# Kernel optimization log

Measured on AMD Instinct MI355X. Metric: run time of the kernel, lower is better.

The kernel has to match this reference:

```python
import jax, jax.numpy as jnp
import numpy as np

EPS = 1e-16


def setup_inputs() -> dict:
    key = jax.random.key(0)
    ks = jax.random.split(key, 7)
    B, N, C = 4096, 2048, 128  # batch of heads, memory rows, memory cols
    k = jax.random.normal(ks[0], (B, C), dtype=jnp.float32)
    beta = jax.random.normal(ks[1], (B, 1), dtype=jnp.float32)
    g = jax.random.normal(ks[2], (B, 1), dtype=jnp.float32)
    s = jax.random.normal(ks[3], (B, 3), dtype=jnp.float32)
    gamma = jax.random.normal(ks[4], (B, 1), dtype=jnp.float32)
    w_prev = jax.random.uniform(ks[5], (B, N), dtype=jnp.float32)
    w_prev = w_prev / jnp.sum(w_prev, axis=1, keepdims=True)  # valid weighting
    M = jax.random.normal(ks[6], (N, C), dtype=jnp.float32)  # memory matrix
    return {"k": k, "beta": beta, "g": g, "s": s, "gamma": gamma,
            "w_prev": w_prev, "M": M}


def reference(k, beta, g, s, gamma, w_prev, M):
    # head activations
    beta = jax.nn.softplus(beta)            # [B,1] key strength > 0
    g = jax.nn.sigmoid(g)                   # [B,1] interpolation gate
    s = jax.nn.softmax(s, axis=-1)          # [B,3] shift distribution
    gamma = 1.0 + jax.nn.softplus(gamma)    # [B,1] sharpening >= 1

    # content addressing: cosine similarity k vs memory rows
    k_norm = jnp.linalg.norm(k, axis=-1, keepdims=True)          # [B,1]
    m_norm = jnp.linalg.norm(M, axis=-1, keepdims=True)          # [N,1]
    sim = jnp.einsum('bc,nc->bn', k, M) / (k_norm * m_norm.T + EPS)  # [B,N]
    w_c = jax.nn.softmax(beta * sim, axis=-1)                    # [B,N]

    # interpolation with previous weighting
    w_g = g * w_c + (1.0 - g) * w_prev                           # [B,N]

    # circular convolution with 3-tap shift kernel (shifts -1, 0, +1)
    w_tilde = (s[:, 0:1] * jnp.roll(w_g, 1, axis=1)
               + s[:, 1:2] * w_g
               + s[:, 2:3] * jnp.roll(w_g, -1, axis=1))          # [B,N]

    # sharpening
    w_sharp = w_tilde ** gamma
    w = w_sharp / (jnp.sum(w_sharp, axis=1, keepdims=True) + EPS)
    return w
```

## Files before the change

kernel.cpp:

```cpp
#include <hip/hip_runtime.h>
#include <math.h>

#define NN 2048
#define CC 128
#define ROWS 16
#define EPSF 1e-16f

typedef __attribute__((ext_vector_type(8))) short bf16x8;
typedef __attribute__((ext_vector_type(4))) float f32x4;

__device__ __forceinline__ float softplusf(float x) {
  return fmaxf(x, 0.0f) + log1pf(__expf(-fabsf(x)));
}

union U8 { uint u[4]; bf16x8 v; };

__device__ __forceinline__ void split8(float4 a, float4 b, bf16x8& hi,
                                       bf16x8& lo, float& sq) {
  float f[8] = {a.x, a.y, a.z, a.w, b.x, b.y, b.z, b.w};
  U8 H, L;
#pragma unroll
  for (int i = 0; i < 4; ++i) {
    float f0 = f[2 * i], f1 = f[2 * i + 1];
    sq += f0 * f0;
    sq += f1 * f1;
    uint u0 = __float_as_uint(f0), u1 = __float_as_uint(f1);
    uint m0 = u0 & 0xffff0000u, m1 = u1 & 0xffff0000u;
    float r0 = f0 - __uint_as_float(m0);
    float r1 = f1 - __uint_as_float(m1);
    H.u[i] = (u0 >> 16) | m1;
    L.u[i] = (__float_as_uint(r0) >> 16) | (__float_as_uint(r1) & 0xffff0000u);
  }
  hi = H.v;
  lo = L.v;
}

__global__ __launch_bounds__(256) void ntm_prep_kernel(
    const float* __restrict__ kptr, const float* __restrict__ beta_,
    const float* __restrict__ g_, const float* __restrict__ s_,
    const float* __restrict__ gamma_, const float* __restrict__ M,
    bf16x8* __restrict__ Mhf, bf16x8* __restrict__ Mlf,
    bf16x8* __restrict__ Khf, bf16x8* __restrict__ Klf,
    float* __restrict__ imn, float* __restrict__ zb, float* __restrict__ gvv,
    float* __restrict__ gmv, float* __restrict__ s0a, float* __restrict__ s1a,
    float* __restrict__ s2a) {
  const int bid = blockIdx.x;
  const int t = threadIdx.x;
  if (bid < 96) {
    const int lane = t & 63;
    const int wv = t >> 6;
    const int l15 = lane & 15;
    const int lg = lane >> 4;
    const bool isM = bid < 32;
    const int grp = (isM ? bid : bid - 32) * 4 + wv;
    const float* src = (isM ? M : kptr) + (grp * 16 + l15) * CC + lg * 8;
    bf16x8* dh = (isM ? Mhf : Khf) + (grp * 4) * 64 + lane;
    bf16x8* dl = (isM ? Mlf : Klf) + (grp * 4) * 64 + lane;
    float sq = 0.f;
#pragma unroll
    for (int ks = 0; ks < 4; ++ks) {
      float4 a0 = *(const float4*)(src + ks * 32);
      float4 a1 = *(const float4*)(src + ks * 32 + 4);
      bf16x8 h, l;
      split8(a0, a1, h, l, sq);
      dh[ks * 64] = h;
      dl[ks * 64] = l;
    }
    sq += __shfl_xor(sq, 16, 64);
    sq += __shfl_xor(sq, 32, 64);
    if (lg == 0) {
      const int row = grp * 16 + l15;
      if (isM) {
        imn[row] = 1.0f / sqrtf(sq);
      } else {
        zb[row] = softplusf(beta_[row]) / sqrtf(sq);
      }
    }
  } else {
    const int r = (bid - 96) * 256 + t;
    gvv[r] = 1.0f / (1.0f + __expf(-g_[r]));
    gmv[r] = 1.0f + softplusf(gamma_[r]);
    float sh0 = s_[3 * r], sh1 = s_[3 * r + 1], sh2 = s_[3 * r + 2];
    float shm = fmaxf(sh0, fmaxf(sh1, sh2));
    float e0 = __expf(sh0 - shm), e1 = __expf(sh1 - shm), e2 = __expf(sh2 - shm);
    float sden = 1.0f / (e0 + e1 + e2);
    s0a[r] = e0 * sden;
    s1a[r] = e1 * sden;
    s2a[r] = e2 * sden;
  }
}

__global__ __launch_bounds__(1024) void ntm_main_kernel(
    const float* __restrict__ w_prev, const bf16x8* __restrict__ Mhf,
    const bf16x8* __restrict__ Mlf, const bf16x8* __restrict__ Khf,
    const bf16x8* __restrict__ Klf, const float* __restrict__ imn,
    const float* __restrict__ zb, const float* __restrict__ gvv,
    const float* __restrict__ gmv, const float* __restrict__ s0a,
    const float* __restrict__ s1a, const float* __restrict__ s2a,
    float* __restrict__ out) {
  __shared__ float red[ROWS][16];
  __shared__ float edges[ROWS][16][2];

  const int t = threadIdx.x;
  const int lane = t & 63;
  const int w = __builtin_amdgcn_readfirstlane(t >> 6);
  const int l15 = lane & 15;
  const int lg = lane >> 4;
  const int bg = blockIdx.x;
  const int b0 = bg * ROWS;

  bf16x8 ah[4], al[4];
#pragma unroll
  for (int ks = 0; ks < 4; ++ks) {
    ah[ks] = Khf[(bg * 4 + ks) * 64 + lane];
    al[ks] = Klf[(bg * 4 + ks) * 64 + lane];
  }

  f32x4 accT[8];
  float imn_t[8];
#pragma unroll
  for (int tt = 0; tt < 8; ++tt) {
    const int gM = 8 * w + tt;
    f32x4 acc = {0.f, 0.f, 0.f, 0.f};
#pragma unroll
    for (int ks = 0; ks < 4; ++ks) {
      bf16x8 bh = Mhf[(gM * 4 + ks) * 64 + lane];
      bf16x8 bl = Mlf[(gM * 4 + ks) * 64 + lane];
      acc = __builtin_amdgcn_mfma_f32_16x16x32_bf16(ah[ks], bh, acc, 0, 0, 0);
      acc = __builtin_amdgcn_mfma_f32_16x16x32_bf16(al[ks], bh, acc, 0, 0, 0);
      acc = __builtin_amdgcn_mfma_f32_16x16x32_bf16(ah[ks], bl, acc, 0, 0, 0);
    }
    accT[tt] = acc;
    imn_t[tt] = imn[128 * w + 16 * tt + l15];
  }

#pragma unroll
  for (int q = 0; q < 4; ++q) {
    const int rr = lg * 4 + q;
    const float zbv = zb[b0 + rr];
    float rs = 0.f;
#pragma unroll
    for (int tt = 0; tt < 8; ++tt) {
      float e = __expf(accT[tt][q] * imn_t[tt] * zbv);
      accT[tt][q] = e;
      rs += e;
    }
    rs += __shfl_xor(rs, 1, 64);
    rs += __shfl_xor(rs, 2, 64);
    rs += __shfl_xor(rs, 4, 64);
    rs += __shfl_xor(rs, 8, 64);
    if (l15 == 0) red[rr][w] = rs;
  }
  __syncthreads();

#pragma unroll
  for (int q = 0; q < 4; ++q) {
    const int rr = lg * 4 + q;
    float4 p0 = *(const float4*)&red[rr][0];
    float4 p1 = *(const float4*)&red[rr][4];
    float4 p2 = *(const float4*)&red[rr][8];
    float4 p3 = *(const float4*)&red[rr][12];
    float tot = (p0.x + p0.y + p0.z + p0.w) + (p1.x + p1.y + p1.z + p1.w) +
                (p2.x + p2.y + p2.z + p2.w) + (p3.x + p3.y + p3.z + p3.w);
    const float gv = gvv[b0 + rr];
    const float ge = gv / tot;
    const float om = 1.0f - gv;
    const size_t rbase = (size_t)(b0 + rr) * NN + 128 * w + l15;
#pragma unroll
    for (int tt = 0; tt < 8; ++tt) {
      float wp = w_prev[rbase + 16 * tt];
      accT[tt][q] = ge * accT[tt][q] + om * wp;
    }
    if (l15 == 0) edges[rr][w][0] = accT[0][q];
    if (l15 == 15) edges[rr][w][1] = accT[7][q];
  }
  __syncthreads();

  const int tm = (lane & 48) | ((lane + 15) & 15);
  const int tp = (lane & 48) | ((lane + 1) & 15);
#pragma unroll
  for (int q = 0; q < 4; ++q) {
    const int rr = lg * 4 + q;
    const float sh0 = s0a[b0 + rr];
    const float sh1 = s1a[b0 + rr];
    const float sh2 = s2a[b0 + rr];
    const float gammav = gmv[b0 + rr];
    const float eL = edges[rr][(w + 15) & 15][1];
    const float eR = edges[rr][(w + 1) & 15][0];

    float sm[8], sp[8];
#pragma unroll
    for (int tt = 0; tt < 8; ++tt) {
      sm[tt] = __shfl(accT[tt][q], tm, 64);
      sp[tt] = __shfl(accT[tt][q], tp, 64);
    }
    float rs = 0.f;
#pragma unroll
    for (int tt = 0; tt < 8; ++tt) {
      float pv = (l15 == 0) ? ((tt == 0) ? eL : sm[tt - 1]) : sm[tt];
      float nx = (l15 == 15) ? ((tt == 7) ? eR : sp[tt + 1]) : sp[tt];
      float wt = sh0 * pv + sh1 * accT[tt][q] + sh2 * nx;
      float p = __expf(gammav * __logf(wt));
      accT[tt][q] = p;
      rs += p;
    }
    rs += __shfl_xor(rs, 1, 64);
    rs += __shfl_xor(rs, 2, 64);
    rs += __shfl_xor(rs, 4, 64);
    rs += __shfl_xor(rs, 8, 64);
    if (l15 == 0) red[rr][w] = rs;
  }
  __syncthreads();

#pragma unroll
  for (int q = 0; q < 4; ++q) {
    const int rr = lg * 4 + q;
    float4 p0 = *(const float4*)&red[rr][0];
    float4 p1 = *(const float4*)&red[rr][4];
    float4 p2 = *(const float4*)&red[rr][8];
    float4 p3 = *(const float4*)&red[rr][12];
    float tot = (p0.x + p0.y + p0.z + p0.w) + (p1.x + p1.y + p1.z + p1.w) +
                (p2.x + p2.y + p2.z + p2.w) + (p3.x + p3.y + p3.z + p3.w);
    const float pinv = 1.0f / (tot + EPSF);
    const size_t rbase = (size_t)(b0 + rr) * NN + 128 * w + l15;
#pragma unroll
    for (int tt = 0; tt < 8; ++tt) {
      out[rbase + 16 * tt] = accT[tt][q] * pinv;
    }
  }
}

__global__ __launch_bounds__(1024) void ntm_main_fallback(
    const float* __restrict__ kptr, const float* __restrict__ beta_,
    const float* __restrict__ g_, const float* __restrict__ s_,
    const float* __restrict__ gamma_, const float* __restrict__ w_prev,
    const float* __restrict__ Mptr, float* __restrict__ out) {
  __shared__ float red[ROWS][16];
  __shared__ float edges[ROWS][16][2];
  const int t = threadIdx.x;
  const int lane = t & 63;
  const int w = __builtin_amdgcn_readfirstlane(t >> 6);
  const int l15 = lane & 15;
  const int lg = lane >> 4;
  const int b0 = blockIdx.x * ROWS;

  const float* kr = kptr + (b0 + l15) * CC + lg * 8;
  bf16x8 ah[4], al[4];
  float ksq = 0.f;
#pragma unroll
  for (int ks = 0; ks < 4; ++ks) {
    float4 a0 = *(const float4*)(kr + ks * 32);
    float4 a1 = *(const float4*)(kr + ks * 32 + 4);
    split8(a0, a1, ah[ks], al[ks], ksq);
  }
  ksq += __shfl_xor(ksq, 16, 64);
  ksq += __shfl_xor(ksq, 32, 64);
  const float ikn_own = 1.0f / sqrtf(ksq);

  f32x4 accT[8];
  float imn[8];
#pragma unroll
  for (int tt = 0; tt < 8; ++tt) {
    const int n0t = 128 * w + 16 * tt;
    const float* mr = Mptr + (size_t)(n0t + l15) * CC + lg * 8;
    f32x4 acc = {0.f, 0.f, 0.f, 0.f};
    float msq = 0.f;
#pragma unroll
    for (int ks = 0; ks < 4; ++ks) {
      float4 m0 = *(const float4*)(mr + ks * 32);
      float4 m1 = *(const float4*)(mr + ks * 32 + 4);
      bf16x8 bh, bl;
      split8(m0, m1, bh, bl, msq);
      acc = __builtin_amdgcn_mfma_f32_16x16x32_bf16(ah[ks], bh, acc, 0, 0, 0);
      acc = __builtin_amdgcn_mfma_f32_16x16x32_bf16(al[ks], bh, acc, 0, 0, 0);
      acc = __builtin_amdgcn_mfma_f32_16x16x32_bf16(ah[ks], bl, acc, 0, 0, 0);
    }
    msq += __shfl_xor(msq, 16, 64);
    msq += __shfl_xor(msq, 32, 64);
    imn[tt] = 1.0f / sqrtf(msq);
    accT[tt] = acc;
  }

#pragma unroll
  for (int q = 0; q < 4; ++q) {
    const int rr = lg * 4 + q;
    const float zb = softplusf(beta_[b0 + rr]) * __shfl(ikn_own, rr, 64);
    float rs = 0.f;
#pragma unroll
    for (int tt = 0; tt < 8; ++tt) {
      float e = __expf(accT[tt][q] * imn[tt] * zb);
      accT[tt][q] = e;
      rs += e;
    }
    rs += __shfl_xor(rs, 1, 64);
    rs += __shfl_xor(rs, 2, 64);
    rs += __shfl_xor(rs, 4, 64);
    rs += __shfl_xor(rs, 8, 64);
    if (l15 == 0) red[rr][w] = rs;
  }
  __syncthreads();

#pragma unroll
  for (int q = 0; q < 4; ++q) {
    const int rr = lg * 4 + q;
    float4 p0 = *(const float4*)&red[rr][0];
    float4 p1 = *(const float4*)&red[rr][4];
    float4 p2 = *(const float4*)&red[rr][8];
    float4 p3 = *(const float4*)&red[rr][12];
    float tot = (p0.x + p0.y + p0.z + p0.w) + (p1.x + p1.y + p1.z + p1.w) +
                (p2.x + p2.y + p2.z + p2.w) + (p3.x + p3.y + p3.z + p3.w);
    const float gv = 1.0f / (1.0f + __expf(-g_[b0 + rr]));
    const float ge = gv / tot;
    const float om = 1.0f - gv;
    const size_t rbase = (size_t)(b0 + rr) * NN + 128 * w + l15;
#pragma unroll
    for (int tt = 0; tt < 8; ++tt) {
      float wp = w_prev[rbase + 16 * tt];
      accT[tt][q] = ge * accT[tt][q] + om * wp;
    }
    if (l15 == 0) edges[rr][w][0] = accT[0][q];
    if (l15 == 15) edges[rr][w][1] = accT[7][q];
  }
  __syncthreads();

  const int tm = (lane & 48) | ((lane + 15) & 15);
  const int tp = (lane & 48) | ((lane + 1) & 15);
#pragma unroll
  for (int q = 0; q < 4; ++q) {
    const int rr = lg * 4 + q;
    float sh0 = s_[3 * (b0 + rr)];
    float sh1 = s_[3 * (b0 + rr) + 1];
    float sh2 = s_[3 * (b0 + rr) + 2];
    float shm = fmaxf(sh0, fmaxf(sh1, sh2));
    float e0 = __expf(sh0 - shm), e1 = __expf(sh1 - shm), e2 = __expf(sh2 - shm);
    float sden = 1.0f / (e0 + e1 + e2);
    sh0 = e0 * sden; sh1 = e1 * sden; sh2 = e2 * sden;
    const float gammav = 1.0f + softplusf(gamma_[b0 + rr]);
    const float eL = edges[rr][(w + 15) & 15][1];
    const float eR = edges[rr][(w + 1) & 15][0];
    float sm[8], sp[8];
#pragma unroll
    for (int tt = 0; tt < 8; ++tt) {
      sm[tt] = __shfl(accT[tt][q], tm, 64);
      sp[tt] = __shfl(accT[tt][q], tp, 64);
    }
    float rs = 0.f;
#pragma unroll
    for (int tt = 0; tt < 8; ++tt) {
      float pv = (l15 == 0) ? ((tt == 0) ? eL : sm[tt - 1]) : sm[tt];
      float nx = (l15 == 15) ? ((tt == 7) ? eR : sp[tt + 1]) : sp[tt];
      float wt = sh0 * pv + sh1 * accT[tt][q] + sh2 * nx;
      float p = __expf(gammav * __logf(wt));
      accT[tt][q] = p;
      rs += p;
    }
    rs += __shfl_xor(rs, 1, 64);
    rs += __shfl_xor(rs, 2, 64);
    rs += __shfl_xor(rs, 4, 64);
    rs += __shfl_xor(rs, 8, 64);
    if (l15 == 0) red[rr][w] = rs;
  }
  __syncthreads();

#pragma unroll
  for (int q = 0; q < 4; ++q) {
    const int rr = lg * 4 + q;
    float4 p0 = *(const float4*)&red[rr][0];
    float4 p1 = *(const float4*)&red[rr][4];
    float4 p2 = *(const float4*)&red[rr][8];
    float4 p3 = *(const float4*)&red[rr][12];
    float tot = (p0.x + p0.y + p0.z + p0.w) + (p1.x + p1.y + p1.z + p1.w) +
                (p2.x + p2.y + p2.z + p2.w) + (p3.x + p3.y + p3.z + p3.w);
    const float pinv = 1.0f / (tot + EPSF);
    const size_t rbase = (size_t)(b0 + rr) * NN + 128 * w + l15;
#pragma unroll
    for (int tt = 0; tt < 8; ++tt) {
      out[rbase + 16 * tt] = accT[tt][q] * pinv;
    }
  }
}

extern "C" void kernel_launch(void* const* d_in, const int* in_sizes, int n_in,
                              void* d_out, int out_size, void* d_ws, size_t ws_size,
                              hipStream_t stream) {
  const float* k = (const float*)d_in[0];
  const float* beta = (const float*)d_in[1];
  const float* g = (const float*)d_in[2];
  const float* s = (const float*)d_in[3];
  const float* gamma = (const float*)d_in[4];
  const float* w_prev = (const float*)d_in[5];
  const float* M = (const float*)d_in[6];
  float* out = (float*)d_out;

  char* ws = (char*)d_ws;
  bf16x8* Mhf = (bf16x8*)(ws + 0);
  bf16x8* Mlf = (bf16x8*)(ws + 524288);
  bf16x8* Khf = (bf16x8*)(ws + 1048576);
  bf16x8* Klf = (bf16x8*)(ws + 2097152);
  float* imn = (float*)(ws + 3145728);
  float* zb = imn + 2048;
  float* gvv = zb + 4096;
  float* gmv = gvv + 4096;
  float* s0a = gmv + 4096;
  float* s1a = s0a + 4096;
  float* s2a = s1a + 4096;
  const size_t need = 3145728 + 2048 * 4 + 6 * 4096 * 4;

  if (ws_size >= need) {
    ntm_prep_kernel<<<112, 256, 0, stream>>>(k, beta, g, s, gamma, M, Mhf, Mlf,
                                             Khf, Klf, imn, zb, gvv, gmv, s0a,
                                             s1a, s2a);
    ntm_main_kernel<<<4096 / ROWS, 1024, 0, stream>>>(
        w_prev, Mhf, Mlf, Khf, Klf, imn, zb, gvv, gmv, s0a, s1a, s2a, out);
  } else {
    ntm_main_fallback<<<4096 / ROWS, 1024, 0, stream>>>(k, beta, g, s, gamma,
                                                        w_prev, M, out);
  }
}
```

Measured before the change: 43.28 us.

## Interleave MFMA chains across tiles and prefetch w_prev before softmax reduction

Reorders the split-bf16 GEMM loop so the k-step is the outer loop and eight independent accumulator tiles are updated per step. This gives the MFMA pipe independent work instead of one serial chain per tile, and all M loads for a k-step are issued together. The w_prev, zb and gate values are loaded right after the GEMM so their latency overlaps the exp/reduction and barrier. The cost is higher register pressure from the 16 bf16x8 B fragments plus 32 w_prev values, which could lower occupancy.

```diff
diff --git a/kernel.cpp b/kernel.cpp
--- a/kernel.cpp
+++ b/kernel.cpp
@@ -109,39 +109,53 @@
   const int bg = blockIdx.x;
   const int b0 = bg * ROWS;
 
-  bf16x8 ah[4], al[4];
+  f32x4 accT[8];
+#pragma unroll
+  for (int tt = 0; tt < 8; ++tt) accT[tt] = (f32x4){0.f, 0.f, 0.f, 0.f};
+
 #pragma unroll
   for (int ks = 0; ks < 4; ++ks) {
-    ah[ks] = Khf[(bg * 4 + ks) * 64 + lane];
-    al[ks] = Klf[(bg * 4 + ks) * 64 + lane];
-  }
-
-  f32x4 accT[8];
+    bf16x8 bh[8], bl[8];
+#pragma unroll
+    for (int tt = 0; tt < 8; ++tt) {
+      const int gM = 8 * w + tt;
+      bh[tt] = Mhf[(gM * 4 + ks) * 64 + lane];
+      bl[tt] = Mlf[(gM * 4 + ks) * 64 + lane];
+    }
+    const bf16x8 ah = Khf[(bg * 4 + ks) * 64 + lane];
+    const bf16x8 al = Klf[(bg * 4 + ks) * 64 + lane];
+#pragma unroll
+    for (int tt = 0; tt < 8; ++tt) {
+      accT[tt] = __builtin_amdgcn_mfma_f32_16x16x32_bf16(ah, bh[tt], accT[tt], 0, 0, 0);
+      accT[tt] = __builtin_amdgcn_mfma_f32_16x16x32_bf16(al, bh[tt], accT[tt], 0, 0, 0);
+      accT[tt] = __builtin_amdgcn_mfma_f32_16x16x32_bf16(ah, bl[tt], accT[tt], 0, 0, 0);
+    }
+  }
+
+  float wp[4][8];
+#pragma unroll
+  for (int q = 0; q < 4; ++q) {
+    const size_t rbase = (size_t)(b0 + lg * 4 + q) * NN + 128 * w + l15;
+#pragma unroll
+    for (int tt = 0; tt < 8; ++tt) wp[q][tt] = w_prev[rbase + 16 * tt];
+  }
   float imn_t[8];
 #pragma unroll
-  for (int tt = 0; tt < 8; ++tt) {
-    const int gM = 8 * w + tt;
-    f32x4 acc = {0.f, 0.f, 0.f, 0.f};
-#pragma unroll
-    for (int ks = 0; ks < 4; ++ks) {
-      bf16x8 bh = Mhf[(gM * 4 + ks) * 64 + lane];
-      bf16x8 bl = Mlf[(gM * 4 + ks) * 64 + lane];
-      acc = __builtin_amdgcn_mfma_f32_16x16x32_bf16(ah[ks], bh, acc, 0, 0, 0);
-      acc = __builtin_amdgcn_mfma_f32_16x16x32_bf16(al[ks], bh, acc, 0, 0, 0);
-      acc = __builtin_amdgcn_mfma_f32_16x16x32_bf16(ah[ks], bl, acc, 0, 0, 0);
-    }
-    accT[tt] = acc;
-    imn_t[tt] = imn[128 * w + 16 * tt + l15];
-  }
-
-#pragma unroll
-  for (int q = 0; q < 4; ++q) {
-    const int rr = lg * 4 + q;
-    const float zbv = zb[b0 + rr];
+  for (int tt = 0; tt < 8; ++tt) imn_t[tt] = imn[128 * w + 16 * tt + l15];
+  float zbv[4], gvq[4];
+#pragma unroll
+  for (int q = 0; q < 4; ++q) {
+    zbv[q] = zb[b0 + lg * 4 + q];
+    gvq[q] = gvv[b0 + lg * 4 + q];
+  }
+
+#pragma unroll
+  for (int q = 0; q < 4; ++q) {
+    const int rr = lg * 4 + q;
     float rs = 0.f;
 #pragma unroll
     for (int tt = 0; tt < 8; ++tt) {
-      float e = __expf(accT[tt][q] * imn_t[tt] * zbv);
+      float e = __expf(accT[tt][q] * imn_t[tt] * zbv[q]);
       accT[tt][q] = e;
       rs += e;
     }
@@ -162,14 +176,12 @@
     float4 p3 = *(const float4*)&red[rr][12];
     float tot = (p0.x + p0.y + p0.z + p0.w) + (p1.x + p1.y + p1.z + p1.w) +
                 (p2.x + p2.y + p2.z + p2.w) + (p3.x + p3.y + p3.z + p3.w);
-    const float gv = gvv[b0 + rr];
+    const float gv = gvq[q];
     const float ge = gv / tot;
     const float om = 1.0f - gv;
-    const size_t rbase = (size_t)(b0 + rr) * NN + 128 * w + l15;
-#pragma unroll
-    for (int tt = 0; tt < 8; ++tt) {
-      float wp = w_prev[rbase + 16 * tt];
-      accT[tt][q] = ge * accT[tt][q] + om * wp;
+#pragma unroll
+    for (int tt = 0; tt < 8; ++tt) {
+      accT[tt][q] = ge * accT[tt][q] + om * wp[q][tt];
     }
     if (l15 == 0) edges[rr][w][0] = accT[0][q];
     if (l15 == 15) edges[rr][w][1] = accT[7][q];
@@ -315,8 +327,8 @@
     const size_t rbase = (size_t)(b0 + rr) * NN + 128 * w + l15;
 #pragma unroll
     for (int tt = 0; tt < 8; ++tt) {
-      float wp = w_prev[rbase + 16 * tt];
-      accT[tt][q] = ge * accT[tt][q] + om * wp;
+      float wpv = w_prev[rbase + 16 * tt];
+      accT[tt][q] = ge * accT[tt][q] + om * wpv;
     }
     if (l15 == 0) edges[rr][w][0] = accT[0][q];
     if (l15 == 15) edges[rr][w][1] = accT[7][q];
```

Result: no change. 42.59 us (-1.6%).

## Split fused NTM kernel into GEMM-exp and row-finish kernels via workspace

Applied to the files above, without the earlier changes.

Replaces the single 1024-thread-per-16-rows kernel with two kernels. The first computes the similarity GEMM and exp for a quarter of the columns per block and writes exp values and partial sums to workspace. The second handles one row per wave to do interpolation, circular shift, sharpening and normalization. This raises block count and parallelism but adds a full B×N intermediate write and read, plus a larger workspace requirement.

```diff
diff --git a/kernel.cpp b/kernel.cpp
--- a/kernel.cpp
+++ b/kernel.cpp
@@ -3,7 +3,6 @@
 
 #define NN 2048
 #define CC 128
-#define ROWS 16
 #define EPSF 1e-16f
 
 typedef __attribute__((ext_vector_type(8))) short bf16x8;
@@ -11,6 +10,11 @@
 
 __device__ __forceinline__ float softplusf(float x) {
   return fmaxf(x, 0.0f) + log1pf(__expf(-fabsf(x)));
+}
+__device__ __forceinline__ float wave_sum(float v) {
+#pragma unroll
+  for (int o = 32; o; o >>= 1) v += __shfl_xor(v, o, 64);
+  return v;
 }
 
 union U8 { uint u[4]; bf16x8 v; };
@@ -90,143 +94,125 @@
   }
 }
 
-__global__ __launch_bounds__(1024) void ntm_main_kernel(
-    const float* __restrict__ w_prev, const bf16x8* __restrict__ Mhf,
-    const bf16x8* __restrict__ Mlf, const bf16x8* __restrict__ Khf,
-    const bf16x8* __restrict__ Klf, const float* __restrict__ imn,
-    const float* __restrict__ zb, const float* __restrict__ gvv,
-    const float* __restrict__ gmv, const float* __restrict__ s0a,
-    const float* __restrict__ s1a, const float* __restrict__ s2a,
-    float* __restrict__ out) {
-  __shared__ float red[ROWS][16];
-  __shared__ float edges[ROWS][16][2];
-
+__global__ __launch_bounds__(256) void ntm_gemm_exp_kernel(
+    const bf16x8* __restrict__ Mhf, const bf16x8* __restrict__ Mlf,
+    const bf16x8* __restrict__ Khf, const bf16x8* __restrict__ Klf,
+    const float* __restrict__ imn, const float* __restrict__ zb,
+    float* __restrict__ ews, float* __restrict__ psum) {
   const int t = threadIdx.x;
   const int lane = t & 63;
   const int w = __builtin_amdgcn_readfirstlane(t >> 6);
   const int l15 = lane & 15;
   const int lg = lane >> 4;
-  const int bg = blockIdx.x;
-  const int b0 = bg * ROWS;
-
-  bf16x8 ah[4], al[4];
+  const int rg = blockIdx.x >> 2;
+  const int cq = blockIdx.x & 3;
+  const int b0 = rg * 16;
+
+  f32x4 accT[8];
+#pragma unroll
+  for (int tt = 0; tt < 8; ++tt) accT[tt] = (f32x4){0.f, 0.f, 0.f, 0.f};
+
 #pragma unroll
   for (int ks = 0; ks < 4; ++ks) {
-    ah[ks] = Khf[(bg * 4 + ks) * 64 + lane];
-    al[ks] = Klf[(bg * 4 + ks) * 64 + lane];
-  }
-
-  f32x4 accT[8];
-  float imn_t[8];
-#pragma unroll
-  for (int tt = 0; tt < 8; ++tt) {
-    const int gM = 8 * w + tt;
-    f32x4 acc = {0.f, 0.f, 0.f, 0.f};
-#pragma unroll
-    for (int ks = 0; ks < 4; ++ks) {
+    const bf16x8 ah = Khf[(rg * 4 + ks) * 64 + lane];
+    const bf16x8 al = Klf[(rg * 4 + ks) * 64 + lane];
+#pragma unroll
+    for (int tt = 0; tt < 8; ++tt) {
+      const int gM = cq * 32 + w * 8 + tt;
       bf16x8 bh = Mhf[(gM * 4 + ks) * 64 + lane];
       bf16x8 bl = Mlf[(gM * 4 + ks) * 64 + lane];
-      acc = __builtin_amdgcn_mfma_f32_16x16x32_bf16(ah[ks], bh, acc, 0, 0, 0);
-      acc = __builtin_amdgcn_mfma_f32_16x16x32_bf16(al[ks], bh, acc, 0, 0, 0);
-      acc = __builtin_amdgcn_mfma_f32_16x16x32_bf16(ah[ks], bl, acc, 0, 0, 0);
-    }
-    accT[tt] = acc;
-    imn_t[tt] = imn[128 * w + 16 * tt + l15];
-  }
+      accT[tt] = __builtin_amdgcn_mfma_f32_16x16x32_bf16(ah, bh, accT[tt], 0, 0, 0);
+      accT[tt] = __builtin_amdgcn_mfma_f32_16x16x32_bf16(al, bh, accT[tt], 0, 0, 0);
+      accT[tt] = __builtin_amdgcn_mfma_f32_16x16x32_bf16(ah, bl, accT[tt], 0, 0, 0);
+    }
+  }
+
+  float imn_t[8];
+#pragma unroll
+  for (int tt = 0; tt < 8; ++tt)
+    imn_t[tt] = imn[cq * 512 + w * 128 + 16 * tt + l15];
 
 #pragma unroll
   for (int q = 0; q < 4; ++q) {
     const int rr = lg * 4 + q;
     const float zbv = zb[b0 + rr];
+    const size_t rbase = (size_t)(b0 + rr) * NN + cq * 512 + w * 128 + l15;
     float rs = 0.f;
 #pragma unroll
     for (int tt = 0; tt < 8; ++tt) {
       float e = __expf(accT[tt][q] * imn_t[tt] * zbv);
-      accT[tt][q] = e;
+      ews[rbase + 16 * tt] = e;
       rs += e;
     }
     rs += __shfl_xor(rs, 1, 64);
     rs += __shfl_xor(rs, 2, 64);
     rs += __shfl_xor(rs, 4, 64);
     rs += __shfl_xor(rs, 8, 64);
-    if (l15 == 0) red[rr][w] = rs;
-  }
-  __syncthreads();
-
-#pragma unroll
-  for (int q = 0; q < 4; ++q) {
-    const int rr = lg * 4 + q;
-    float4 p0 = *(const float4*)&red[rr][0];
-    float4 p1 = *(const float4*)&red[rr][4];
-    float4 p2 = *(const float4*)&red[rr][8];
-    float4 p3 = *(const float4*)&red[rr][12];
-    float tot = (p0.x + p0.y + p0.z + p0.w) + (p1.x + p1.y + p1.z + p1.w) +
-                (p2.x + p2.y + p2.z + p2.w) + (p3.x + p3.y + p3.z + p3.w);
-    const float gv = gvv[b0 + rr];
-    const float ge = gv / tot;
-    const float om = 1.0f - gv;
-    const size_t rbase = (size_t)(b0 + rr) * NN + 128 * w + l15;
-#pragma unroll
-    for (int tt = 0; tt < 8; ++tt) {
-      float wp = w_prev[rbase + 16 * tt];
-      accT[tt][q] = ge * accT[tt][q] + om * wp;
-    }
-    if (l15 == 0) edges[rr][w][0] = accT[0][q];
-    if (l15 == 15) edges[rr][w][1] = accT[7][q];
-  }
-  __syncthreads();
-
-  const int tm = (lane & 48) | ((lane + 15) & 15);
-  const int tp = (lane & 48) | ((lane + 1) & 15);
-#pragma unroll
-  for (int q = 0; q < 4; ++q) {
-    const int rr = lg * 4 + q;
-    const float sh0 = s0a[b0 + rr];
-    const float sh1 = s1a[b0 + rr];
-    const float sh2 = s2a[b0 + rr];
-    const float gammav = gmv[b0 + rr];
-    const float eL = edges[rr][(w + 15) & 15][1];
-    const float eR = edges[rr][(w + 1) & 15][0];
-
-    float sm[8], sp[8];
-#pragma unroll
-    for (int tt = 0; tt < 8; ++tt) {
-      sm[tt] = __shfl(accT[tt][q], tm, 64);
-      sp[tt] = __shfl(accT[tt][q], tp, 64);
-    }
-    float rs = 0.f;
-#pragma unroll
-    for (int tt = 0; tt < 8; ++tt) {
-      float pv = (l15 == 0) ? ((tt == 0) ? eL : sm[tt - 1]) : sm[tt];
-      float nx = (l15 == 15) ? ((tt == 7) ? eR : sp[tt + 1]) : sp[tt];
-      float wt = sh0 * pv + sh1 * accT[tt][q] + sh2 * nx;
-      float p = __expf(gammav * __logf(wt));
-      accT[tt][q] = p;
-      rs += p;
-    }
-    rs += __shfl_xor(rs, 1, 64);
-    rs += __shfl_xor(rs, 2, 64);
-    rs += __shfl_xor(rs, 4, 64);
-    rs += __shfl_xor(rs, 8, 64);
-    if (l15 == 0) red[rr][w] = rs;
-  }
-  __syncthreads();
-
-#pragma unroll
-  for (int q = 0; q < 4; ++q) {
-    const int rr = lg * 4 + q;
-    float4 p0 = *(const float4*)&red[rr][0];
-    float4 p1 = *(const float4*)&red[rr][4];
-    float4 p2 = *(const float4*)&red[rr][8];
-    float4 p3 = *(const float4*)&red[rr][12];
-    float tot = (p0.x + p0.y + p0.z + p0.w) + (p1.x + p1.y + p1.z + p1.w) +
-                (p2.x + p2.y + p2.z + p2.w) + (p3.x + p3.y + p3.z + p3.w);
-    const float pinv = 1.0f / (tot + EPSF);
-    const size_t rbase = (size_t)(b0 + rr) * NN + 128 * w + l15;
-#pragma unroll
-    for (int tt = 0; tt < 8; ++tt) {
-      out[rbase + 16 * tt] = accT[tt][q] * pinv;
-    }
+    if (l15 == 0) psum[(size_t)(b0 + rr) * 16 + cq * 4 + w] = rs;
+  }
+}
+
+__global__ __launch_bounds__(256) void ntm_finish_kernel(
+    const float* __restrict__ ews, const float* __restrict__ psum,
+    const float* __restrict__ w_prev, const float* __restrict__ gvv,
+    const float* __restrict__ gmv, const float* __restrict__ s0a,
+    const float* __restrict__ s1a, const float* __restrict__ s2a,
+    float* __restrict__ out) {
+  const int t = threadIdx.x;
+  const int lane = t & 63;
+  const int wv = __builtin_amdgcn_readfirstlane(t >> 6);
+  const int row = blockIdx.x * 4 + wv;
+  const int lanem1 = (lane + 63) & 63;
+  const int lanep1 = (lane + 1) & 63;
+
+  const float* pp = psum + (size_t)row * 16;
+  float tot = 0.f;
+#pragma unroll
+  for (int j = 0; j < 4; ++j) {
+    float4 p = *(const float4*)(pp + 4 * j);
+    tot += (p.x + p.y) + (p.z + p.w);
+  }
+  const float gv = gvv[row];
+  const float ge = gv / tot;
+  const float om = 1.0f - gv;
+  const float sh0 = s0a[row];
+  const float sh1 = s1a[row];
+  const float sh2 = s2a[row];
+  const float gammav = gmv[row];
+
+  const size_t rbase = (size_t)row * NN + lane;
+
+  float wg[32];
+#pragma unroll
+  for (int li = 0; li < 32; ++li) {
+    float e = ews[rbase + 64 * li];
+    float wp = w_prev[rbase + 64 * li];
+    wg[li] = ge * e + om * wp;
+  }
+
+  float a_prev = __shfl(wg[31], lanem1, 64);
+  float b_cur = __shfl(wg[0], lanep1, 64);
+  const float b_wrap = b_cur;
+  float sp = 0.f;
+#pragma unroll
+  for (int li = 0; li < 32; ++li) {
+    float a_cur = __shfl(wg[li], lanem1, 64);
+    float b_next = (li < 31) ? __shfl(wg[(li + 1) & 31], lanep1, 64) : b_wrap;
+    float pv = (lane == 0) ? a_prev : a_cur;
+    float nx = (lane == 63) ? b_next : b_cur;
+    float wt = sh0 * pv + sh1 * wg[li] + sh2 * nx;
+    float p = __expf(gammav * __logf(wt));
+    wg[li] = p;
+    sp += p;
+    a_prev = a_cur;
+    b_cur = b_next;
+  }
+  sp = wave_sum(sp);
+  const float pinv = 1.0f / (sp + EPSF);
+
+#pragma unroll
+  for (int li = 0; li < 32; ++li) {
+    out[rbase + 64 * li] = wg[li] * pinv;
   }
 }
 
@@ -235,14 +221,14 @@
     const float* __restrict__ g_, const float* __restrict__ s_,
     const float* __restrict__ gamma_, const float* __restrict__ w_prev,
     const float* __restrict__ Mptr, float* __restrict__ out) {
-  __shared__ float red[ROWS][16];
-  __shared__ float edges[ROWS][16][2];
+  __shared__ float red[16][16];
+  __shared__ float edges[16][16][2];
   const int t = threadIdx.x;
   const int lane = t & 63;
   const int w = __builtin_amdgcn_readfirstlane(t >> 6);
   const int l15 = lane & 15;
   const int lg = lane >> 4;
-  const int b0 = blockIdx.x * ROWS;
+  const int b0 = blockIdx.x * 16;
 
   const float* kr = kptr + (b0 + l15) * CC + lg * 8;
   bf16x8 ah[4], al[4];
@@ -315,8 +301,8 @@
     const size_t rbase = (size_t)(b0 + rr) * NN + 128 * w + l15;
 #pragma unroll
     for (int tt = 0; tt < 8; ++tt) {
-      float wp = w_prev[rbase + 16 * tt];
-      accT[tt][q] = ge * accT[tt][q] + om * wp;
+      float wpv = w_prev[rbase + 16 * tt];
+      accT[tt][q] = ge * accT[tt][q] + om * wpv;
     }
     if (l15 == 0) edges[rr][w][0] = accT[0][q];
     if (l15 == 15) edges[rr][w][1] = accT[7][q];
@@ -404,16 +390,20 @@
   float* s0a = gmv + 4096;
   float* s1a = s0a + 4096;
   float* s2a = s1a + 4096;
-  const size_t need = 3145728 + 2048 * 4 + 6 * 4096 * 4;
+  float* ews = (float*)(ws + (4 << 20));
+  float* psum = (float*)(ws + (36 << 20));
+  const size_t need = (36 << 20) + 4096 * 16 * 4;
 
   if (ws_size >= need) {
     ntm_prep_kernel<<<112, 256, 0, stream>>>(k, beta, g, s, gamma, M, Mhf, Mlf,
                                              Khf, Klf, imn, zb, gvv, gmv, s0a,
                                              s1a, s2a);
-    ntm_main_kernel<<<4096 / ROWS, 1024, 0, stream>>>(
-        w_prev, Mhf, Mlf, Khf, Klf, imn, zb, gvv, gmv, s0a, s1a, s2a, out);
+    ntm_gemm_exp_kernel<<<1024, 256, 0, stream>>>(Mhf, Mlf, Khf, Klf, imn, zb,
+                                                  ews, psum);
+    ntm_finish_kernel<<<1024, 256, 0, stream>>>(ews, psum, w_prev, gvv, gmv,
+                                                s0a, s1a, s2a, out);
   } else {
-    ntm_main_fallback<<<4096 / ROWS, 1024, 0, stream>>>(k, beta, g, s, gamma,
-                                                        w_prev, M, out);
-  }
-}
+    ntm_main_fallback<<<4096 / 16, 1024, 0, stream>>>(k, beta, g, s, gamma,
+                                                      w_prev, M, out);
+  }
+}
```

Measured after the change: 49.17 us. +13.6%, slower.

## Split each 16-row block across two workgroups and batch M-fragment loads

Applied to the files above, without the earlier changes.

The main kernel now launches 512 blocks instead of 256. Each pair of blocks recomputes the same 16x2048 MFMA similarity tile, and each block handles only two of the four accumulator rows per lane group in the softmax, interpolation, shift/sharpen and store phases. The MFMA loop is reordered to load all eight M fragments per k-step before issuing the MFMAs, and the w_prev loads are hoisted ahead of the first reduction. This aims to fill more CUs with only 256 blocks and to hide memory latency, at the cost of doing the matmul and reading M twice.

```diff
diff --git a/kernel.cpp b/kernel.cpp
--- a/kernel.cpp
+++ b/kernel.cpp
@@ -3,7 +3,6 @@
 
 #define NN 2048
 #define CC 128
-#define ROWS 16
 #define EPSF 1e-16f
 
 typedef __attribute__((ext_vector_type(8))) short bf16x8;
@@ -98,8 +97,8 @@
     const float* __restrict__ gmv, const float* __restrict__ s0a,
     const float* __restrict__ s1a, const float* __restrict__ s2a,
     float* __restrict__ out) {
-  __shared__ float red[ROWS][16];
-  __shared__ float edges[ROWS][16][2];
+  __shared__ float red[16][16];
+  __shared__ float edges[16][16][2];
 
   const int t = threadIdx.x;
   const int lane = t & 63;
@@ -107,127 +106,147 @@
   const int l15 = lane & 15;
   const int lg = lane >> 4;
   const int bg = blockIdx.x;
-  const int b0 = bg * ROWS;
+  const int kg = bg >> 1;
+  const int half = bg & 1;
+  const int b0 = kg * 16;
 
   bf16x8 ah[4], al[4];
 #pragma unroll
   for (int ks = 0; ks < 4; ++ks) {
-    ah[ks] = Khf[(bg * 4 + ks) * 64 + lane];
-    al[ks] = Klf[(bg * 4 + ks) * 64 + lane];
+    ah[ks] = Khf[(kg * 4 + ks) * 64 + lane];
+    al[ks] = Klf[(kg * 4 + ks) * 64 + lane];
   }
 
   f32x4 accT[8];
+#pragma unroll
+  for (int tt = 0; tt < 8; ++tt) accT[tt] = (f32x4){0.f, 0.f, 0.f, 0.f};
+
+#pragma unroll
+  for (int ks = 0; ks < 4; ++ks) {
+    bf16x8 bh[8], bl[8];
+#pragma unroll
+    for (int tt = 0; tt < 8; ++tt) {
+      const int gM = 8 * w + tt;
+      bh[tt] = Mhf[(gM * 4 + ks) * 64 + lane];
+      bl[tt] = Mlf[(gM * 4 + ks) * 64 + lane];
+    }
+#pragma unroll
+    for (int tt = 0; tt < 8; ++tt) {
+      accT[tt] = __builtin_amdgcn_mfma_f32_16x16x32_bf16(ah[ks], bh[tt], accT[tt], 0, 0, 0);
+      accT[tt] = __builtin_amdgcn_mfma_f32_16x16x32_bf16(al[ks], bh[tt], accT[tt], 0, 0, 0);
+      accT[tt] = __builtin_amdgcn_mfma_f32_16x16x32_bf16(ah[ks], bl[tt], accT[tt], 0, 0, 0);
+    }
+  }
+
   float imn_t[8];
 #pragma unroll
-  for (int tt = 0; tt < 8; ++tt) {
-    const int gM = 8 * w + tt;
-    f32x4 acc = {0.f, 0.f, 0.f, 0.f};
-#pragma unroll
-    for (int ks = 0; ks < 4; ++ks) {
-      bf16x8 bh = Mhf[(gM * 4 + ks) * 64 + lane];
-      bf16x8 bl = Mlf[(gM * 4 + ks) * 64 + lane];
-      acc = __builtin_amdgcn_mfma_f32_16x16x32_bf16(ah[ks], bh, acc, 0, 0, 0);
-      acc = __builtin_amdgcn_mfma_f32_16x16x32_bf16(al[ks], bh, acc, 0, 0, 0);
-      acc = __builtin_amdgcn_mfma_f32_16x16x32_bf16(ah[ks], bl, acc, 0, 0, 0);
-    }
-    accT[tt] = acc;
-    imn_t[tt] = imn[128 * w + 16 * tt + l15];
-  }
-
-#pragma unroll
-  for (int q = 0; q < 4; ++q) {
-    const int rr = lg * 4 + q;
-    const float zbv = zb[b0 + rr];
-    float rs = 0.f;
-#pragma unroll
-    for (int tt = 0; tt < 8; ++tt) {
-      float e = __expf(accT[tt][q] * imn_t[tt] * zbv);
-      accT[tt][q] = e;
-      rs += e;
-    }
-    rs += __shfl_xor(rs, 1, 64);
-    rs += __shfl_xor(rs, 2, 64);
-    rs += __shfl_xor(rs, 4, 64);
-    rs += __shfl_xor(rs, 8, 64);
-    if (l15 == 0) red[rr][w] = rs;
-  }
-  __syncthreads();
-
-#pragma unroll
-  for (int q = 0; q < 4; ++q) {
-    const int rr = lg * 4 + q;
-    float4 p0 = *(const float4*)&red[rr][0];
-    float4 p1 = *(const float4*)&red[rr][4];
-    float4 p2 = *(const float4*)&red[rr][8];
-    float4 p3 = *(const float4*)&red[rr][12];
-    float tot = (p0.x + p0.y + p0.z + p0.w) + (p1.x + p1.y + p1.z + p1.w) +
-                (p2.x + p2.y + p2.z + p2.w) + (p3.x + p3.y + p3.z + p3.w);
-    const float gv = gvv[b0 + rr];
-    const float ge = gv / tot;
-    const float om = 1.0f - gv;
+  for (int tt = 0; tt < 8; ++tt) imn_t[tt] = imn[128 * w + 16 * tt + l15];
+
+  float wp[2][8];
+  float zbv[2], gvq[2];
+#pragma unroll
+  for (int qi = 0; qi < 2; ++qi) {
+    const int rr = lg * 4 + 2 * half + qi;
     const size_t rbase = (size_t)(b0 + rr) * NN + 128 * w + l15;
 #pragma unroll
-    for (int tt = 0; tt < 8; ++tt) {
-      float wp = w_prev[rbase + 16 * tt];
-      accT[tt][q] = ge * accT[tt][q] + om * wp;
-    }
-    if (l15 == 0) edges[rr][w][0] = accT[0][q];
-    if (l15 == 15) edges[rr][w][1] = accT[7][q];
-  }
+    for (int tt = 0; tt < 8; ++tt) wp[qi][tt] = w_prev[rbase + 16 * tt];
+    zbv[qi] = zb[b0 + rr];
+    gvq[qi] = gvv[b0 + rr];
+  }
+
+#define PH2A(Q, QI)                                                       \
+  {                                                                       \
+    const int rr = lg * 4 + (Q);                                          \
+    float rs = 0.f;                                                       \
+    _Pragma("unroll") for (int tt = 0; tt < 8; ++tt) {                    \
+      float e = __expf(accT[tt][(Q)] * imn_t[tt] * zbv[(QI)]);            \
+      accT[tt][(Q)] = e;                                                  \
+      rs += e;                                                            \
+    }                                                                     \
+    rs += __shfl_xor(rs, 1, 64);                                          \
+    rs += __shfl_xor(rs, 2, 64);                                          \
+    rs += __shfl_xor(rs, 4, 64);                                          \
+    rs += __shfl_xor(rs, 8, 64);                                          \
+    if (l15 == 0) red[rr][w] = rs;                                        \
+  }
+  if (half) { PH2A(2, 0); PH2A(3, 1); } else { PH2A(0, 0); PH2A(1, 1); }
+#undef PH2A
+  __syncthreads();
+
+#define PH2B(Q, QI)                                                       \
+  {                                                                       \
+    const int rr = lg * 4 + (Q);                                          \
+    float4 p0 = *(const float4*)&red[rr][0];                              \
+    float4 p1 = *(const float4*)&red[rr][4];                              \
+    float4 p2 = *(const float4*)&red[rr][8];                              \
+    float4 p3 = *(const float4*)&red[rr][12];                             \
+    float tot = (p0.x + p0.y + p0.z + p0.w) + (p1.x + p1.y + p1.z + p1.w) \
+              + (p2.x + p2.y + p2.z + p2.w) + (p3.x + p3.y + p3.z + p3.w);\
+    const float gv = gvq[(QI)];                                           \
+    const float ge = gv / tot;                                            \
+    const float om = 1.0f - gv;                                           \
+    _Pragma("unroll") for (int tt = 0; tt < 8; ++tt) {                    \
+      accT[tt][(Q)] = ge * accT[tt][(Q)] + om * wp[(QI)][tt];             \
+    }                                                                     \
+    if (l15 == 0) edges[rr][w][0] = accT[0][(Q)];                         \
+    if (l15 == 15) edges[rr][w][1] = accT[7][(Q)];                        \
+  }
+  if (half) { PH2B(2, 0); PH2B(3, 1); } else { PH2B(0, 0); PH2B(1, 1); }
+#undef PH2B
   __syncthreads();
 
   const int tm = (lane & 48) | ((lane + 15) & 15);
   const int tp = (lane & 48) | ((lane + 1) & 15);
-#pragma unroll
-  for (int q = 0; q < 4; ++q) {
-    const int rr = lg * 4 + q;
-    const float sh0 = s0a[b0 + rr];
-    const float sh1 = s1a[b0 + rr];
-    const float sh2 = s2a[b0 + rr];
-    const float gammav = gmv[b0 + rr];
-    const float eL = edges[rr][(w + 15) & 15][1];
-    const float eR = edges[rr][(w + 1) & 15][0];
-
-    float sm[8], sp[8];
-#pragma unroll
-    for (int tt = 0; tt < 8; ++tt) {
-      sm[tt] = __shfl(accT[tt][q], tm, 64);
-      sp[tt] = __shfl(accT[tt][q], tp, 64);
-    }
-    float rs = 0.f;
-#pragma unroll
-    for (int tt = 0; tt < 8; ++tt) {
-      float pv = (l15 == 0) ? ((tt == 0) ? eL : sm[tt - 1]) : sm[tt];
-      float nx = (l15 == 15) ? ((tt == 7) ? eR : sp[tt + 1]) : sp[tt];
-      float wt = sh0 * pv + sh1 * accT[tt][q] + sh2 * nx;
-      float p = __expf(gammav * __logf(wt));
-      accT[tt][q] = p;
-      rs += p;
-    }
-    rs += __shfl_xor(rs, 1, 64);
-    rs += __shfl_xor(rs, 2, 64);
-    rs += __shfl_xor(rs, 4, 64);
-    rs += __shfl_xor(rs, 8, 64);
-    if (l15 == 0) red[rr][w] = rs;
-  }
-  __syncthreads();
-
-#pragma unroll
-  for (int q = 0; q < 4; ++q) {
-    const int rr = lg * 4 + q;
-    float4 p0 = *(const float4*)&red[rr][0];
-    float4 p1 = *(const float4*)&red[rr][4];
-    float4 p2 = *(const float4*)&red[rr][8];
-    float4 p3 = *(const float4*)&red[rr][12];
-    float tot = (p0.x + p0.y + p0.z + p0.w) + (p1.x + p1.y + p1.z + p1.w) +
-                (p2.x + p2.y + p2.z + p2.w) + (p3.x + p3.y + p3.z + p3.w);
-    const float pinv = 1.0f / (tot + EPSF);
-    const size_t rbase = (size_t)(b0 + rr) * NN + 128 * w + l15;
-#pragma unroll
-    for (int tt = 0; tt < 8; ++tt) {
-      out[rbase + 16 * tt] = accT[tt][q] * pinv;
-    }
-  }
+#define PH2C(Q, QI)                                                       \
+  {                                                                       \
+    const int rr = lg * 4 + (Q);                                          \
+    const float sh0 = s0a[b0 + rr];                                       \
+    const float sh1 = s1a[b0 + rr];                                       \
+    const float sh2 = s2a[b0 + rr];                                       \
+    const float gammav = gmv[b0 + rr];                                    \
+    const float eL = edges[rr][(w + 15) & 15][1];                         \
+    const float eR = edges[rr][(w + 1) & 15][0];                          \
+    float sm[8], sp[8];                                                   \
+    _Pragma("unroll") for (int tt = 0; tt < 8; ++tt) {                    \
+      sm[tt] = __shfl(accT[tt][(Q)], tm, 64);                             \
+      sp[tt] = __shfl(accT[tt][(Q)], tp, 64);                             \
+    }                                                                     \
+    float rs = 0.f;                                                       \
+    _Pragma("unroll") for (int tt = 0; tt < 8; ++tt) {                    \
+      float pv = (l15 == 0) ? ((tt == 0) ? eL : sm[tt - 1]) : sm[tt];     \
+      float nx = (l15 == 15) ? ((tt == 7) ? eR : sp[tt + 1]) : sp[tt];    \
+      float wt = sh0 * pv + sh1 * accT[tt][(Q)] + sh2 * nx;               \
+      float p = __expf(gammav * __logf(wt));                              \
+      accT[tt][(Q)] = p;                                                  \
+      rs += p;                                                            \
+    }                                                                     \
+    rs += __shfl_xor(rs, 1, 64);                                          \
+    rs += __shfl_xor(rs, 2, 64);                                          \
+    rs += __shfl_xor(rs, 4, 64);                                          \
+    rs += __shfl_xor(rs, 8, 64);                                          \
+    if (l15 == 0) red[rr][w] = rs;                                        \
+  }
+  if (half) { PH2C(2, 0); PH2C(3, 1); } else { PH2C(0, 0); PH2C(1, 1); }
+#undef PH2C
+  __syncthreads();
+
+#define PH2D(Q, QI)                                                       \
+  {                                                                       \
+    const int rr = lg * 4 + (Q);                                          \
+    float4 p0 = *(const float4*)&red[rr][0];                              \
+    float4 p1 = *(const float4*)&red[rr][4];                              \
+    float4 p2 = *(const float4*)&red[rr][8];                              \
+    float4 p3 = *(const float4*)&red[rr][12];                             \
+    float tot = (p0.x + p0.y + p0.z + p0.w) + (p1.x + p1.y + p1.z + p1.w) \
+              + (p2.x + p2.y + p2.z + p2.w) + (p3.x + p3.y + p3.z + p3.w);\
+    const float pinv = 1.0f / (tot + EPSF);                               \
+    const size_t rbase = (size_t)(b0 + rr) * NN + 128 * w + l15;          \
+    _Pragma("unroll") for (int tt = 0; tt < 8; ++tt) {                    \
+      out[rbase + 16 * tt] = accT[tt][(Q)] * pinv;                        \
+    }                                                                     \
+  }
+  if (half) { PH2D(2, 0); PH2D(3, 1); } else { PH2D(0, 0); PH2D(1, 1); }
+#undef PH2D
 }
 
 __global__ __launch_bounds__(1024) void ntm_main_fallback(
@@ -235,14 +254,14 @@
     const float* __restrict__ g_, const float* __restrict__ s_,
     const float* __restrict__ gamma_, const float* __restrict__ w_prev,
     const float* __restrict__ Mptr, float* __restrict__ out) {
-  __shared__ float red[ROWS][16];
-  __shared__ float edges[ROWS][16][2];
+  __shared__ float red[16][16];
+  __shared__ float edges[16][16][2];
   const int t = threadIdx.x;
   const int lane = t & 63;
   const int w = __builtin_amdgcn_readfirstlane(t >> 6);
   const int l15 = lane & 15;
   const int lg = lane >> 4;
-  const int b0 = blockIdx.x * ROWS;
+  const int b0 = blockIdx.x * 16;
 
   const float* kr = kptr + (b0 + l15) * CC + lg * 8;
   bf16x8 ah[4], al[4];
@@ -315,8 +334,8 @@
     const size_t rbase = (size_t)(b0 + rr) * NN + 128 * w + l15;
 #pragma unroll
     for (int tt = 0; tt < 8; ++tt) {
-      float wp = w_prev[rbase + 16 * tt];
-      accT[tt][q] = ge * accT[tt][q] + om * wp;
+      float wpv = w_prev[rbase + 16 * tt];
+      accT[tt][q] = ge * accT[tt][q] + om * wpv;
     }
     if (l15 == 0) edges[rr][w][0] = accT[0][q];
     if (l15 == 15) edges[rr][w][1] = accT[7][q];
@@ -410,10 +429,10 @@
     ntm_prep_kernel<<<112, 256, 0, stream>>>(k, beta, g, s, gamma, M, Mhf, Mlf,
                                              Khf, Klf, imn, zb, gvv, gmv, s0a,
                                              s1a, s2a);
-    ntm_main_kernel<<<4096 / ROWS, 1024, 0, stream>>>(
-        w_prev, Mhf, Mlf, Khf, Klf, imn, zb, gvv, gmv, s0a, s1a, s2a, out);
+    ntm_main_kernel<<<512, 1024, 0, stream>>>(w_prev, Mhf, Mlf, Khf, Klf, imn,
+                                              zb, gvv, gmv, s0a, s1a, s2a, out);
   } else {
-    ntm_main_fallback<<<4096 / ROWS, 1024, 0, stream>>>(k, beta, g, s, gamma,
-                                                        w_prev, M, out);
-  }
-}
+    ntm_main_fallback<<<256, 1024, 0, stream>>>(k, beta, g, s, gamma, w_prev,
+                                                M, out);
+  }
+}
```

Result: slower. 56.55 us (+30.7%).
